# Kernel optimization log

Measured on AMD Instinct MI355X. Metric: run time of the kernel, lower is better.

## Reference

```python
import jax, jax.numpy as jnp
import numpy as np
import math

HIDDEN = 2048
NUM_HEADS = 16
HEAD_DIM = HIDDEN // NUM_HEADS  # 128
BATCH = 2
SEQ = 2048


def setup_inputs() -> dict:
    key = jax.random.key(0)
    ks = jax.random.split(key, 9)
    s = 1.0 / math.sqrt(HIDDEN)
    x = jax.random.normal(ks[0], (BATCH, SEQ, HIDDEN), dtype=jnp.float32)
    # weights stored [in, out] (transpose of torch Linear weight)
    Wq = jax.random.uniform(ks[1], (HIDDEN, HIDDEN), jnp.float32, -s, s)
    bq = jax.random.uniform(ks[2], (HIDDEN,), jnp.float32, -s, s)
    Wk = jax.random.uniform(ks[3], (HIDDEN, HEAD_DIM), jnp.float32, -s, s)
    bk = jax.random.uniform(ks[4], (HEAD_DIM,), jnp.float32, -s, s)
    Wv = jax.random.uniform(ks[5], (HIDDEN, HEAD_DIM), jnp.float32, -s, s)
    bv = jax.random.uniform(ks[6], (HEAD_DIM,), jnp.float32, -s, s)
    Wo = jax.random.uniform(ks[7], (HIDDEN, HIDDEN), jnp.float32, -s, s)
    bo = jax.random.uniform(ks[8], (HIDDEN,), jnp.float32, -s, s)
    return {"x": x, "Wq": Wq, "bq": bq, "Wk": Wk, "bk": bk,
            "Wv": Wv, "bv": bv, "Wo": Wo, "bo": bo}


def reference(x, Wq, bq, Wk, bk, Wv, bv, Wo, bo):
    B, S, _ = x.shape
    scale = 1.0 / math.sqrt(HEAD_DIM)
    q = (x @ Wq + bq).reshape(B, S, NUM_HEADS, HEAD_DIM)  # [B,S,H,D]
    k = x @ Wk + bk  # [B,S,D] single shared KV head
    v = x @ Wv + bv  # [B,S,D]
    # scores: [B,H,S,S]
    scores = jnp.einsum('bqhd,bkd->bhqk', q, k) * scale
    w = jax.nn.softmax(scores, axis=-1)
    # dropout p=0.0 (eval-equivalent): identity
    o = jnp.einsum('bhqk,bkd->bqhd', w, v).reshape(B, S, HIDDEN)
    return o @ Wo + bo
```

## Files before the change

kernel.cpp:

```cpp
#include <hip/hip_runtime.h>
#include <stdint.h>

#define H_   2048
#define NH   16
#define HD   128
#define B_   2
#define S_   2048
#define NR   (B_*S_)
#define NQKV (H_ + 2*HD)

typedef __attribute__((ext_vector_type(8))) short bf16x8;
typedef __attribute__((ext_vector_type(4))) float f32x4;
typedef __attribute__((ext_vector_type(16))) float f32x16;
typedef __attribute__((ext_vector_type(4))) unsigned short u16x4;

#define MFMA(a,b,c) __builtin_amdgcn_mfma_f32_16x16x32_bf16(a,b,c,0,0,0)
#define MFMA32(a,b,c) __builtin_amdgcn_mfma_f32_32x32x16_bf16(a,b,c,0,0,0)
#define PLSWAP(a,b) asm("v_permlane32_swap_b32 %0, %1" : "+v"(a), "+v"(b))

__device__ __forceinline__ unsigned short f2bf(float f){
  union{ float f; unsigned int u; } v; v.f = f;
  unsigned int u = v.u;
  return (unsigned short)((u + 0x7fffu + ((u>>16)&1u)) >> 16);
}
__device__ __forceinline__ float bf2f(unsigned short u){
  union{ unsigned int i; float f; } v; v.i = (unsigned int)u << 16; return v.f;
}
__device__ __forceinline__ unsigned int cvtpk(float lo, float hi){
  unsigned int r;
  asm("v_cvt_pk_bf16_f32 %0, %1, %2" : "=v"(r) : "v"(lo), "v"(hi));
  return r;
}

__device__ __forceinline__ void gl_lds16(const void* g, void* l){
  __builtin_amdgcn_global_load_lds((const __attribute__((address_space(1))) void*)g,
                                   (__attribute__((address_space(3))) void*)l, 16, 0, 0);
}

__global__ __launch_bounds__(256) void k_convx(const float* __restrict__ x,
                                               unsigned short* __restrict__ xb){
  long i = ((long)blockIdx.x*256 + threadIdx.x)*4;
  float4 f = *reinterpret_cast<const float4*>(x + i);
  u16x4 o;
  o[0]=f2bf(f.x); o[1]=f2bf(f.y); o[2]=f2bf(f.z); o[3]=f2bf(f.w);
  *reinterpret_cast<u16x4*>(xb + i) = o;
}

__global__ __launch_bounds__(256) void k_transw(const float* __restrict__ W,
                                                unsigned short* __restrict__ Bt,
                                                int N, int rowoff){
  __shared__ float t[32][33];
  int n0 = blockIdx.x*32, k0 = blockIdx.y*32;
  int tx = threadIdx.x & 31, ty = threadIdx.x >> 5;
  #pragma unroll
  for(int r=0;r<32;r+=8) t[ty+r][tx] = W[(long)(k0+ty+r)*N + n0+tx];
  __syncthreads();
  #pragma unroll
  for(int r=0;r<32;r+=8)
    Bt[(long)(rowoff + n0+ty+r)*2048 + k0+tx] = f2bf(t[tx][ty+r]);
}

__global__ __launch_bounds__(256) void k_transv(const unsigned short* __restrict__ QKV,
                                                unsigned short* __restrict__ Vtg){
  __shared__ unsigned short t[32][33];
  int s0 = blockIdx.x*32, d0 = blockIdx.y*32, z = blockIdx.z;
  int tx = threadIdx.x & 31, ty = threadIdx.x >> 5;
  #pragma unroll
  for(int r=0;r<32;r+=8)
    t[ty+r][tx] = QKV[(long)(z*S_ + s0+ty+r)*NQKV + (H_+HD) + d0+tx];
  __syncthreads();
  #pragma unroll
  for(int r=0;r<32;r+=8)
    Vtg[(long)z*HD*S_ + (long)(d0+ty+r)*S_ + s0+tx] = t[tx][ty+r];
}

template<int OUT_BF16>
__global__ __launch_bounds__(256) void k_gemm(const unsigned short* __restrict__ A,
                                              const unsigned short* __restrict__ Bt,
                                              const float* __restrict__ b0,
                                              const float* __restrict__ b1,
                                              const float* __restrict__ b2,
                                              void* __restrict__ out,
                                              int M, int N, int K){
  __shared__ unsigned short lA[2][128*64];
  __shared__ unsigned short lB[2][128*64];
  const int tid = threadIdx.x, lane = tid & 63, w = tid >> 6;
  const int wr = w >> 1, wc = w & 1;
  int flat = blockIdx.y*gridDim.x + blockIdx.x;
  { int cpx = (gridDim.x*gridDim.y) >> 3; flat = (flat & 7)*cpx + (flat >> 3); }
  const long bm = (long)(flat / gridDim.x)*128, bn = (long)(flat % gridDim.x)*128;
  const int rl = lane & 15, rh = lane >> 4;
  f32x4 acc[4][4] = {};

  const int scb = ((lane & 7) ^ (lane >> 3)) * 8;
  long arow[4], brow[4];
  #pragma unroll
  for(int q=0;q<4;q++){
    int r8 = (w*4+q)*8 + (lane>>3);
    arow[q] = bm + r8; brow[q] = bn + r8;
  }

  auto stage = [&](int kt, int buf){
    const int k0 = kt << 6;
    #pragma unroll
    for(int q=0;q<4;q++){
      gl_lds16(A  + arow[q]*K + k0 + scb, &lA[buf][(w*4+q)*512]);
      gl_lds16(Bt + brow[q]*K + k0 + scb, &lB[buf][(w*4+q)*512]);
    }
  };

  const int nk = K >> 6;
  stage(0, 0);
  __syncthreads();

  for(int kt=0; kt<nk; ++kt){
    const int cur = kt & 1;
    if(kt+1 < nk) stage(kt+1, cur^1);
    #pragma unroll
    for(int kk=0;kk<2;kk++){
      bf16x8 af[4], bfr[4];
      #pragma unroll
      for(int i=0;i<4;i++){
        int ra = wr*64 + i*16 + rl;
        af[i]  = *(const bf16x8*)((const char*)&lA[cur][0] + ra*128 + (((rh + kk*4) ^ (rl&7))<<4));
        int rb = wc*64 + i*16 + rl;
        bfr[i] = *(const bf16x8*)((const char*)&lB[cur][0] + rb*128 + (((rh + kk*4) ^ (rl&7))<<4));
      }
      #pragma unroll
      for(int i=0;i<4;i++)
        #pragma unroll
        for(int j=0;j<4;j++)
          acc[i][j] = MFMA(af[i], bfr[j], acc[i][j]);
    }
    __syncthreads();
  }

  #pragma unroll
  for(int j=0;j<4;j++){
    long col = bn + wc*64 + j*16 + rl;
    float bb;
    if(col < 2048)      bb = b0[col];
    else if(col < 2176) bb = b1[col-2048];
    else                bb = b2[col-2176];
    #pragma unroll
    for(int i=0;i<4;i++){
      long row = bm + wr*64 + i*16 + rh*4;
      #pragma unroll
      for(int r=0;r<4;r++){
        float v = acc[i][j][r] + bb;
        if(OUT_BF16) ((unsigned short*)out)[(row+r)*N + col] = f2bf(v);
        else         ((float*)out)[(row+r)*N + col] = v;
      }
    }
  }
}

__global__ __launch_bounds__(256) void k_attn(const unsigned short* __restrict__ QKV,
                                              const unsigned short* __restrict__ Vtg,
                                              unsigned short* __restrict__ OpA,
                                              unsigned short* __restrict__ OpB,
                                              float* __restrict__ lbuf){
  const int qt = blockIdx.x, h = blockIdx.y;
  const int b = blockIdx.z >> 1, half = blockIdx.z & 1;
  const int tid = threadIdx.x, lane = tid & 63, w = tid >> 6;
  const int ql = lane & 31, hi = lane >> 5;
  const int swl = ql & 15;
  const int swv = (ql >> 1) & 3;
  __shared__ char lds[34816];
  const float C1 = 0.12751746f;

  const long qrow = (long)b*S_ + qt*128 + w*32 + ql;
  bf16x8 qf[8];
  #pragma unroll
  for(int kk=0;kk<8;kk++)
    qf[kk] = *(const bf16x8*)&QKV[qrow*NQKV + h*HD + kk*16 + hi*8];

  f32x16 oacc[4] = {};
  float lrun = 0.f;

  const char* Kg = (const char*)QKV + (long)b*S_*4608 + 4096 + (long)half*1024*4608;
  const char* Vt = (const char*)Vtg + (long)b*HD*S_*2 + half*2048;

  int koff[8];
  #pragma unroll
  for(int kk=0;kk<8;kk++) koff[kk] = ql*256 + (((kk*2+hi) ^ swl)*16);
  int voff[2][4];
  #pragma unroll
  for(int kk=0;kk<2;kk++)
    #pragma unroll
    for(int d32=0;d32<4;d32++)
      voff[kk][d32] = (d32*32+ql)*64 + (((kk*2+hi) ^ swv)*16);

  const int krA = (w*2+0)*4 + (lane>>4), krB = (w*2+1)*4 + (lane>>4);
  const int vrA = (w*2+0)*16 + (lane>>2), vrB = (w*2+1)*16 + (lane>>2);
  const char* kpA = Kg + (long)krA*4608 + (((lane&15) ^ (krA&15))*16);
  const char* kpB = Kg + (long)krB*4608 + (((lane&15) ^ (krB&15))*16);
  const char* vpA = Vt + (long)vrA*4096 + (((lane&3) ^ ((vrA>>1)&3))*16);
  const char* vpB = Vt + (long)vrB*4096 + (((lane&3) ^ ((vrB>>1)&3))*16);

#define ATTN_STAGE(BUF) do{                                                   \
    gl_lds16(kpA, lds + (BUF)*16384 + (w*2+0)*1024);                          \
    gl_lds16(kpB, lds + (BUF)*16384 + (w*2+1)*1024);                          \
    gl_lds16(vpA, lds + (BUF)*16384 + 8192 + (w*2+0)*1024);                   \
    gl_lds16(vpB, lds + (BUF)*16384 + 8192 + (w*2+1)*1024);                   \
    kpA += 32*4608; kpB += 32*4608; vpA += 64; vpB += 64;                     \
  }while(0)

#define ATTN_TILE(CUR, DO_STAGE) do{                                          \
    if(DO_STAGE) ATTN_STAGE((CUR)^1);                                         \
    const char* kc = lds + (CUR)*16384;                                       \
    const char* vc = kc + 8192;                                               \
    f32x16 sacc = {};                                                         \
    _Pragma("unroll")                                                         \
    for(int g=0; g<2; g++){                                                   \
      bf16x8 kf[4];                                                           \
      _Pragma("unroll")                                                       \
      for(int j=0;j<4;j++) kf[j] = *(const bf16x8*)(kc + koff[g*4+j]);        \
      _Pragma("unroll")                                                       \
      for(int j=0;j<4;j++) sacc = MFMA32(kf[j], qf[g*4+j], sacc);             \
    }                                                                         \
    float ps0=0.f, ps1=0.f, ps2=0.f, ps3=0.f;                                 \
    _Pragma("unroll")                                                         \
    for(int r=0;r<16;r+=4){                                                   \
      float p0=__builtin_exp2f(sacc[r]*C1),   p1=__builtin_exp2f(sacc[r+1]*C1);\
      float p2=__builtin_exp2f(sacc[r+2]*C1), p3=__builtin_exp2f(sacc[r+3]*C1);\
      sacc[r]=p0; sacc[r+1]=p1; sacc[r+2]=p2; sacc[r+3]=p3;                   \
      ps0+=p0; ps1+=p1; ps2+=p2; ps3+=p3;                                     \
    }                                                                         \
    lrun += (ps0+ps1)+(ps2+ps3);                                              \
    bf16x8 pa[2];                                                             \
    {                                                                         \
      unsigned int k0m0 = cvtpk(sacc[0],  sacc[1]),  k0m1 = cvtpk(sacc[2],  sacc[3]);  \
      unsigned int k1m0 = cvtpk(sacc[4],  sacc[5]),  k1m1 = cvtpk(sacc[6],  sacc[7]);  \
      unsigned int k2m0 = cvtpk(sacc[8],  sacc[9]),  k2m1 = cvtpk(sacc[10], sacc[11]); \
      unsigned int k3m0 = cvtpk(sacc[12], sacc[13]), k3m1 = cvtpk(sacc[14], sacc[15]); \
      PLSWAP(k0m0, k1m0); PLSWAP(k0m1, k1m1);                                 \
      PLSWAP(k2m0, k3m0); PLSWAP(k2m1, k3m1);                                 \
      union { unsigned int u[4]; bf16x8 v; } f0, f1;                          \
      f0.u[0]=k0m0; f0.u[1]=k0m1; f0.u[2]=k1m0; f0.u[3]=k1m1;                 \
      f1.u[0]=k2m0; f1.u[1]=k2m1; f1.u[2]=k3m0; f1.u[3]=k3m1;                 \
      pa[0] = f0.v; pa[1] = f1.v;                                             \
    }                                                                         \
    _Pragma("unroll")                                                         \
    for(int kk=0;kk<2;kk++){                                                  \
      bf16x8 vf[4];                                                           \
      _Pragma("unroll")                                                       \
      for(int d32=0; d32<4; d32++) vf[d32] = *(const bf16x8*)(vc + voff[kk][d32]); \
      _Pragma("unroll")                                                       \
      for(int d32=0; d32<4; d32++) oacc[d32] = MFMA32(vf[d32], pa[kk], oacc[d32]); \
    }                                                                         \
    __syncthreads();                                                          \
  }while(0)

  ATTN_STAGE(0);
  __syncthreads();

  for(int it=0; it<16; ++it){
    ATTN_TILE(0, true);
    ATTN_TILE(1, it != 15);
  }

#undef ATTN_TILE
#undef ATTN_STAGE

  lrun += __shfl_xor(lrun, 32);
  const float linv = 1.0f / lrun;
  unsigned short* Odst = half ? OpB : OpA;
  unsigned short* ot = (unsigned short*)(lds) + w*(128*34);
  #pragma unroll
  for(int d32=0; d32<4; d32++)
    #pragma unroll
    for(int r=0;r<16;r++){
      int d = d32*32 + (r&3) + 8*(r>>2) + 4*hi;
      ot[d*34 + ql] = f2bf(oacc[d32][r]*linv);
    }
  unsigned short* dst = Odst + qrow*H_ + h*HD + hi*64;
  #pragma unroll
  for(int i=0;i<8;i++){
    union { unsigned short s[8]; bf16x8 v; } o;
    #pragma unroll
    for(int e=0;e<8;e++) o.s[e] = ot[(hi*64 + i*8 + e)*34 + ql];
    *(bf16x8*)(dst + i*8) = o.v;
  }
  if(hi == 0)
    lbuf[(long)half*65536 + qrow*16 + h] = lrun;
}

__global__ __launch_bounds__(256) void k_merge(unsigned short* __restrict__ OpA,
                                               const unsigned short* __restrict__ OpB,
                                               const float* __restrict__ lbuf){
  long idx = (long)blockIdx.x*256 + threadIdx.x;
  long row = idx >> 8;
  int  c8  = (int)(idx & 255);
  int  h   = c8 >> 4;
  float la = lbuf[row*16 + h];
  float lb = lbuf[65536 + row*16 + h];
  float dn = 1.0f/(la + lb);
  float fa = la*dn, fb = lb*dn;
  union { unsigned short s[8]; bf16x8 v; } va, vb, o;
  va.v = *(const bf16x8*)(OpA + row*2048 + c8*8);
  vb.v = *(const bf16x8*)(OpB + row*2048 + c8*8);
  #pragma unroll
  for(int e=0;e<8;e++)
    o.s[e] = f2bf(bf2f(va.s[e])*fa + bf2f(vb.s[e])*fb);
  *(bf16x8*)(OpA + row*2048 + c8*8) = o.v;
}

extern "C" void kernel_launch(void* const* d_in, const int* in_sizes, int n_in,
                              void* d_out, int out_size, void* d_ws, size_t ws_size,
                              hipStream_t stream){
  (void)in_sizes; (void)n_in; (void)out_size; (void)ws_size;
  const float* x  = (const float*)d_in[0];
  const float* Wq = (const float*)d_in[1];
  const float* bq = (const float*)d_in[2];
  const float* Wk = (const float*)d_in[3];
  const float* bk = (const float*)d_in[4];
  const float* Wv = (const float*)d_in[5];
  const float* bv = (const float*)d_in[6];
  const float* Wo = (const float*)d_in[7];
  const float* bo = (const float*)d_in[8];
  float* out = (float*)d_out;

  char* wsb = (char*)d_ws;
  size_t off = 0;
  auto alloc = [&](size_t bytes){ void* p = wsb + off; off += (bytes + 255) & ~(size_t)255; return p; };
  unsigned short* xb   = (unsigned short*)alloc((size_t)NR*H_*2);
  unsigned short* Bqkv = (unsigned short*)alloc((size_t)NQKV*H_*2);
  unsigned short* Wot  = (unsigned short*)alloc((size_t)H_*H_*2);
  unsigned short* QKV  = (unsigned short*)alloc((size_t)NR*NQKV*2);
  unsigned short* Vtg  = (unsigned short*)alloc((size_t)B_*HD*S_*2);
  unsigned short* Ob   = (unsigned short*)alloc((size_t)NR*H_*2);
  unsigned short* OpB  = xb;
  float*          lbuf = (float*)Bqkv;

  k_convx  <<<NR*H_/1024, 256, 0, stream>>>(x, xb);
  k_transw <<<dim3(64,64), 256, 0, stream>>>(Wq, Bqkv, H_, 0);
  k_transw <<<dim3(4,64),  256, 0, stream>>>(Wk, Bqkv, HD, H_);
  k_transw <<<dim3(4,64),  256, 0, stream>>>(Wv, Bqkv, HD, H_+HD);
  k_transw <<<dim3(64,64), 256, 0, stream>>>(Wo, Wot, H_, 0);

  k_gemm<1><<<dim3(NQKV/128, NR/128), 256, 0, stream>>>(xb, Bqkv, bq, bk, bv, QKV, NR, NQKV, H_);
  k_transv <<<dim3(S_/32, HD/32, B_), 256, 0, stream>>>(QKV, Vtg);
  k_attn   <<<dim3(S_/128, NH, B_*2), 256, 0, stream>>>(QKV, Vtg, Ob, OpB, lbuf);
  k_merge  <<<NR*H_/8/256, 256, 0, stream>>>(Ob, OpB, lbuf);
  k_gemm<0><<<dim3(H_/128, NR/128), 256, 0, stream>>>(Ob, Wot, bo, bo, bo, out, NR, H_, H_);
}
```

Before: 222.7 us.

## Halve attention block size to 64 query rows and merge weight transpose launches

The attention kernel now uses 128 threads covering 64 query rows per block, with each wave staging four K/V chunks per tile, which doubles the grid and is meant to raise occupancy and balance across CUs. The four weight-transpose launches are fused into one 3D-grid kernel to cut launch overhead. In exchange, each K/V tile is reused by fewer query rows, raising L2/global load traffic per unit of work, and the LDS allocation shrinks.

```diff
diff --git a/kernel.cpp b/kernel.cpp
--- a/kernel.cpp
+++ b/kernel.cpp
@@ -46,11 +46,21 @@
   *reinterpret_cast<u16x4*>(xb + i) = o;
 }
 
-__global__ __launch_bounds__(256) void k_transw(const float* __restrict__ W,
-                                                unsigned short* __restrict__ Bt,
-                                                int N, int rowoff){
+__global__ __launch_bounds__(256) void k_transw4(const float* __restrict__ Wq,
+                                                 const float* __restrict__ Wk,
+                                                 const float* __restrict__ Wv,
+                                                 const float* __restrict__ Wo,
+                                                 unsigned short* __restrict__ Bqkv,
+                                                 unsigned short* __restrict__ Wot){
   __shared__ float t[32][33];
-  int n0 = blockIdx.x*32, k0 = blockIdx.y*32;
+  const int z = blockIdx.z;
+  const float* W; unsigned short* Bt; int N, rowoff, xx;
+  if(blockIdx.x < 64){
+    W = z ? Wo : Wq; Bt = z ? Wot : Bqkv; N = H_; rowoff = 0; xx = blockIdx.x;
+  } else {
+    W = z ? Wv : Wk; Bt = Bqkv; N = HD; rowoff = z ? (H_+HD) : H_; xx = blockIdx.x - 64;
+  }
+  int n0 = xx*32, k0 = blockIdx.y*32;
   int tx = threadIdx.x & 31, ty = threadIdx.x >> 5;
   #pragma unroll
   for(int r=0;r<32;r+=8) t[ty+r][tx] = W[(long)(k0+ty+r)*N + n0+tx];
@@ -155,7 +165,7 @@
   }
 }
 
-__global__ __launch_bounds__(256) void k_attn(const unsigned short* __restrict__ QKV,
+__global__ __launch_bounds__(128) void k_attn(const unsigned short* __restrict__ QKV,
                                               const unsigned short* __restrict__ Vtg,
                                               unsigned short* __restrict__ OpA,
                                               unsigned short* __restrict__ OpB,
@@ -166,10 +176,10 @@
   const int ql = lane & 31, hi = lane >> 5;
   const int swl = ql & 15;
   const int swv = (ql >> 1) & 3;
-  __shared__ char lds[34816];
+  __shared__ char lds[32768];
   const float C1 = 0.12751746f;
 
-  const long qrow = (long)b*S_ + qt*128 + w*32 + ql;
+  const long qrow = (long)b*S_ + qt*64 + w*32 + ql;
   bf16x8 qf[8];
   #pragma unroll
   for(int kk=0;kk<8;kk++)
@@ -191,19 +201,23 @@
     for(int d32=0;d32<4;d32++)
       voff[kk][d32] = (d32*32+ql)*64 + (((kk*2+hi) ^ swv)*16);
 
-  const int krA = (w*2+0)*4 + (lane>>4), krB = (w*2+1)*4 + (lane>>4);
-  const int vrA = (w*2+0)*16 + (lane>>2), vrB = (w*2+1)*16 + (lane>>2);
-  const char* kpA = Kg + (long)krA*4608 + (((lane&15) ^ (krA&15))*16);
-  const char* kpB = Kg + (long)krB*4608 + (((lane&15) ^ (krB&15))*16);
-  const char* vpA = Vt + (long)vrA*4096 + (((lane&3) ^ ((vrA>>1)&3))*16);
-  const char* vpB = Vt + (long)vrB*4096 + (((lane&3) ^ ((vrB>>1)&3))*16);
+  const char* kp[4]; const char* vp[4];
+  #pragma unroll
+  for(int j=0;j<4;j++){
+    int g = w*4 + j;
+    int kr = g*4 + (lane>>4);
+    kp[j] = Kg + (long)kr*4608 + (((lane&15) ^ (kr&15))*16);
+    int vr = g*16 + (lane>>2);
+    vp[j] = Vt + (long)vr*4096 + (((lane&3) ^ ((vr>>1)&3))*16);
+  }
 
 #define ATTN_STAGE(BUF) do{                                                   \
-    gl_lds16(kpA, lds + (BUF)*16384 + (w*2+0)*1024);                          \
-    gl_lds16(kpB, lds + (BUF)*16384 + (w*2+1)*1024);                          \
-    gl_lds16(vpA, lds + (BUF)*16384 + 8192 + (w*2+0)*1024);                   \
-    gl_lds16(vpB, lds + (BUF)*16384 + 8192 + (w*2+1)*1024);                   \
-    kpA += 32*4608; kpB += 32*4608; vpA += 64; vpB += 64;                     \
+    _Pragma("unroll")                                                         \
+    for(int j=0;j<4;j++){                                                     \
+      gl_lds16(kp[j], lds + (BUF)*16384 + (w*4+j)*1024);                      \
+      gl_lds16(vp[j], lds + (BUF)*16384 + 8192 + (w*4+j)*1024);               \
+      kp[j] += 32*4608; vp[j] += 64;                                          \
+    }                                                                         \
   }while(0)
 
 #define ATTN_TILE(CUR, DO_STAGE) do{                                          \
@@ -212,12 +226,11 @@
     const char* vc = kc + 8192;                                               \
     f32x16 sacc = {};                                                         \
     _Pragma("unroll")                                                         \
-    for(int g=0; g<2; g++){                                                   \
-      bf16x8 kf[4];                                                           \
-      _Pragma("unroll")                                                       \
-      for(int j=0;j<4;j++) kf[j] = *(const bf16x8*)(kc + koff[g*4+j]);        \
-      _Pragma("unroll")                                                       \
-      for(int j=0;j<4;j++) sacc = MFMA32(kf[j], qf[g*4+j], sacc);             \
+    for(int g=0; g<4; g++){                                                   \
+      bf16x8 kf0 = *(const bf16x8*)(kc + koff[g*2]);                          \
+      bf16x8 kf1 = *(const bf16x8*)(kc + koff[g*2+1]);                        \
+      sacc = MFMA32(kf0, qf[g*2], sacc);                                      \
+      sacc = MFMA32(kf1, qf[g*2+1], sacc);                                    \
     }                                                                         \
     float ps0=0.f, ps1=0.f, ps2=0.f, ps3=0.f;                                 \
     _Pragma("unroll")                                                         \
@@ -243,11 +256,13 @@
     }                                                                         \
     _Pragma("unroll")                                                         \
     for(int kk=0;kk<2;kk++){                                                  \
-      bf16x8 vf[4];                                                           \
       _Pragma("unroll")                                                       \
-      for(int d32=0; d32<4; d32++) vf[d32] = *(const bf16x8*)(vc + voff[kk][d32]); \
-      _Pragma("unroll")                                                       \
-      for(int d32=0; d32<4; d32++) oacc[d32] = MFMA32(vf[d32], pa[kk], oacc[d32]); \
+      for(int dp=0; dp<2; dp++){                                              \
+        bf16x8 vf0 = *(const bf16x8*)(vc + voff[kk][dp*2]);                   \
+        bf16x8 vf1 = *(const bf16x8*)(vc + voff[kk][dp*2+1]);                 \
+        oacc[dp*2]   = MFMA32(vf0, pa[kk], oacc[dp*2]);                       \
+        oacc[dp*2+1] = MFMA32(vf1, pa[kk], oacc[dp*2+1]);                     \
+      }                                                                       \
     }                                                                         \
     __syncthreads();                                                          \
   }while(0)
@@ -334,14 +349,11 @@
   float*          lbuf = (float*)Bqkv;
 
   k_convx  <<<NR*H_/1024, 256, 0, stream>>>(x, xb);
-  k_transw <<<dim3(64,64), 256, 0, stream>>>(Wq, Bqkv, H_, 0);
-  k_transw <<<dim3(4,64),  256, 0, stream>>>(Wk, Bqkv, HD, H_);
-  k_transw <<<dim3(4,64),  256, 0, stream>>>(Wv, Bqkv, HD, H_+HD);
-  k_transw <<<dim3(64,64), 256, 0, stream>>>(Wo, Wot, H_, 0);
+  k_transw4<<<dim3(68,64,2), 256, 0, stream>>>(Wq, Wk, Wv, Wo, Bqkv, Wot);
 
   k_gemm<1><<<dim3(NQKV/128, NR/128), 256, 0, stream>>>(xb, Bqkv, bq, bk, bv, QKV, NR, NQKV, H_);
   k_transv <<<dim3(S_/32, HD/32, B_), 256, 0, stream>>>(QKV, Vtg);
-  k_attn   <<<dim3(S_/128, NH, B_*2), 256, 0, stream>>>(QKV, Vtg, Ob, OpB, lbuf);
+  k_attn   <<<dim3(S_/64, NH, B_*2), 128, 0, stream>>>(QKV, Vtg, Ob, OpB, lbuf);
   k_merge  <<<NR*H_/8/256, 256, 0, stream>>>(Ob, OpB, lbuf);
   k_gemm<0><<<dim3(H_/128, NR/128), 256, 0, stream>>>(Ob, Wot, bo, bo, bo, out, NR, H_, H_);
 }
```

New measurement: 232.3 us. +4.3%, slower.
